# Kernel optimization log

Measured on AMD Instinct MI355X. Metric: run time of the kernel, lower is better.

## Reference

```python
import jax, jax.numpy as jnp
import numpy as np

BN_EPS = 1e-5


def conv1x1(x, W, b):
    # x: [B, Cin, N], W: [Cout, Cin], b: [Cout]
    return jnp.einsum('oc,bcn->bon', W, x) + b[None, :, None]


def bn(x, p):
    # p: [4, C] rows = gamma, beta, running_mean, running_var (inference BN)
    g, be, m, v = p[0], p[1], p[2], p[3]
    inv = jax.lax.rsqrt(v + BN_EPS)
    return (x - m[None, :, None]) * (g * inv)[None, :, None] + be[None, :, None]


def conv_bn_relu(x, W, b, p):
    return jax.nn.relu(bn(conv1x1(x, W, b), p))


def _make_params(key, cout, cin):
    k1, k2 = jax.random.split(key)
    W = jax.random.normal(k1, (cout, cin), jnp.float32) * (1.0 / np.sqrt(cin))
    b = jax.random.normal(k2, (cout,), jnp.float32) * 0.01
    p = jnp.stack([jnp.ones(cout), jnp.zeros(cout), jnp.zeros(cout), jnp.ones(cout)]).astype(jnp.float32)
    return W, b, p


def setup_inputs() -> dict:
    key = jax.random.key(0)
    ks = jax.random.split(key, 16)
    B, N, S, D1, D2 = 2, 16384, 4096, 128, 256
    Cin, C, Cm = D1 + D2 + 13, 128, 128  # 397, out_channel, mlp[0]
    inp = {
        'xyz1': jax.random.normal(ks[0], (B, N, 3), jnp.float32),
        'xyz2': jax.random.normal(ks[1], (B, S, 3), jnp.float32),
        'points1': jax.random.normal(ks[2], (B, D1, N), jnp.float32),
        'points2': jax.random.normal(ks[3], (B, D2, S), jnp.float32),
        'last_pred': jax.random.normal(ks[4], (B, S, 13), jnp.float32),
    }
    inp['fuse_W'], inp['fuse_b'], inp['fuse_bn'] = _make_params(ks[5], C, Cin)
    inp['ext1_W'], inp['ext1_b'], inp['ext1_bn'] = _make_params(ks[6], C, C)
    inp['ext2_W'], inp['ext2_b'], inp['ext2_bn'] = _make_params(ks[7], C, C)
    inp['pred1_W'], inp['pred1_b'], inp['pred1_bn'] = _make_params(ks[8], Cm, C)
    inp['pred2_W'], inp['pred2_b'], inp['pred2_bn'] = _make_params(ks[9], 13, Cm)
    return inp


def _forward(xyz1, xyz2, points1, points2, last_pred,
             fuse_W, fuse_b, fuse_bn, ext1_W, ext1_b, ext1_bn,
             ext2_W, ext2_b, ext2_bn, pred1_W, pred1_b, pred1_bn,
             pred2_W, pred2_b, pred2_bn):
    B, N, _ = xyz1.shape
    p1 = jnp.transpose(points1, (0, 2, 1))  # [B, N, D1]
    p2 = jnp.transpose(points2, (0, 2, 1))  # [B, S, D2]
    # squared distances [B, N, S]
    dists = (jnp.sum(xyz1 ** 2, -1)[:, :, None]
             + jnp.sum(xyz2 ** 2, -1)[:, None, :]
             - 2.0 * jnp.einsum('bnc,bsc->bns', xyz1, xyz2))
    # 3 smallest distances (partial top-k instead of full sort; same math)
    neg_d3, idx = jax.lax.top_k(-dists, 3)  # [B, N, 3]
    d3 = -neg_d3
    recip = 1.0 / (d3 + 1e-8)
    weight = recip / jnp.sum(recip, axis=2, keepdims=True)  # [B, N, 3]
    bidx = jnp.arange(B)[:, None, None]
    interp_pts = jnp.sum(p2[bidx, idx] * weight[..., None], axis=2)        # [B, N, D2]
    interp_pred = jnp.sum(last_pred[bidx, idx] * weight[..., None], axis=2)  # [B, N, 13]
    new_points = jnp.transpose(jnp.concatenate([p1, interp_pts, interp_pred], axis=-1), (0, 2, 1))  # [B, Cin, N]
    # fuse
    x = conv_bn_relu(new_points, fuse_W, fuse_b, fuse_bn)
    # extraction: one ConvBNReLURes1D block (groups=1, res_expansion=1)
    h = conv_bn_relu(x, ext1_W, ext1_b, ext1_bn)
    x = jax.nn.relu(bn(conv1x1(h, ext2_W, ext2_b), ext2_bn) + x)  # [B, C, N]
    new_points_out = x
    # prediction head (dropout is identity in eval mode)
    feat = conv_bn_relu(x, pred1_W, pred1_b, pred1_bn)
    pred = conv_bn_relu(feat, pred2_W, pred2_b, pred2_bn)
    return (new_points_out,
            jnp.transpose(feat, (0, 2, 1)),
            jnp.transpose(pred, (0, 2, 1)))


def reference(xyz1, xyz2, points1, points2, last_pred,
              fuse_W, fuse_b, fuse_bn, ext1_W, ext1_b, ext1_bn,
              ext2_W, ext2_b, ext2_bn, pred1_W, pred1_b, pred1_bn,
              pred2_W, pred2_b, pred2_bn):
    return _forward(xyz1, xyz2, points1, points2, last_pred,
                    fuse_W, fuse_b, fuse_bn, ext1_W, ext1_b, ext1_bn,
                    ext2_W, ext2_b, ext2_bn, pred1_W, pred1_b, pred1_bn,
                    pred2_W, pred2_b, pred2_bn)
```

## Files before the change

### kernel.cpp

```cpp
#include <hip/hip_runtime.h>
#include <stdint.h>

#define B_   2
#define N_   16384
#define S_   4096
#define D2_  256
#define CIN_ 397
#define KP_  416
#define C_   128
#define OC_  13
#define NCHUNK_ 16
#define CHS_ (S_ / NCHUNK_)
#define NCAND_ (NCHUNK_ * 3)
#define XBI_P 296

typedef unsigned short u16;
typedef unsigned int u32;
typedef short s16x8 __attribute__((ext_vector_type(8)));
typedef float f32x4 __attribute__((ext_vector_type(4)));

#define MFMA16(a, b, c) __builtin_amdgcn_mfma_f32_16x16x32_bf16((a), (b), (c), 0, 0, 0)

__device__ __forceinline__ float b2f(u16 h) {
  union { unsigned int u; float f; } v; v.u = ((unsigned int)h) << 16; return v.f;
}
__device__ __forceinline__ u16 f2b(float f) {
  union { float f; unsigned int u; } v; v.f = f;
  unsigned int r = v.u + 0x7fffu + ((v.u >> 16) & 1u);
  return (u16)(r >> 16);
}

__global__ void prep_kernel(const float* __restrict__ fW, const float* __restrict__ fb,
                            const float* __restrict__ fbn,
                            const float* __restrict__ e1W, const float* __restrict__ e1b,
                            const float* __restrict__ e1bn,
                            const float* __restrict__ e2W, const float* __restrict__ e2b,
                            const float* __restrict__ e2bn,
                            const float* __restrict__ p1W, const float* __restrict__ p1b,
                            const float* __restrict__ p1bn,
                            const float* __restrict__ p2W, const float* __restrict__ p2b,
                            const float* __restrict__ p2bn,
                            u16* __restrict__ Wf, u16* __restrict__ W1o,
                            u16* __restrict__ W2o, u16* __restrict__ W3o,
                            u16* __restrict__ Wp2, float* __restrict__ st) {
  int tid = blockIdx.x * 256 + threadIdx.x;
  int stride = gridDim.x * 256;
  for (int i = tid; i < 128 * KP_; i += stride) {
    int m = i / KP_, k = i - m * KP_;
    Wf[i] = (k < CIN_) ? f2b(fW[m * CIN_ + k]) : (u16)0;
  }
  for (int i = tid; i < 128 * 128; i += stride) {
    W1o[i] = f2b(e1W[i]);
    W2o[i] = f2b(e2W[i]);
    W3o[i] = f2b(p1W[i]);
  }
  for (int i = tid; i < 16 * 128; i += stride) {
    int m = i >> 7;
    Wp2[i] = (m < OC_) ? f2b(p2W[i]) : (u16)0;
  }
  for (int i = tid; i < 5 * 128; i += stride) {
    int sg = i >> 7, c = i & 127;
    const float* bn; const float* bc; int Cc = 128;
    switch (sg) {
      case 0: bn = fbn;  bc = fb;  break;
      case 1: bn = e1bn; bc = e1b; break;
      case 2: bn = e2bn; bc = e2b; break;
      case 3: bn = p1bn; bc = p1b; break;
      default: bn = p2bn; bc = p2b; Cc = OC_; break;
    }
    float s = 0.f, t = 0.f;
    if (c < Cc) {
      float g  = bn[0 * Cc + c], be = bn[1 * Cc + c];
      float mu = bn[2 * Cc + c], vv = bn[3 * Cc + c];
      float inv = 1.0f / sqrtf(vv + 1e-5f);
      s = g * inv;
      t = (bc[c] - mu) * s + be;
    }
    st[sg * 256 + c] = s;
    st[sg * 256 + 128 + c] = t;
  }
}

__global__ void transpose_f2b_kernel(const float* __restrict__ in, u16* __restrict__ out,
                                     int C, int S, int opitch) {
  __shared__ float tile[64][65];
  int b = blockIdx.z;
  int s0 = blockIdx.x * 64, c0 = blockIdx.y * 64;
  const float* ip = in + (size_t)b * C * S;
  u16* op = out + (size_t)b * S * opitch;
  int tr = threadIdx.x >> 4;
  int tc4 = (threadIdx.x & 15) * 4;
#pragma unroll
  for (int r = 0; r < 64; r += 16) {
    float4 v = *(const float4*)(ip + (size_t)(c0 + tr + r) * S + s0 + tc4);
    tile[tr + r][tc4 + 0] = v.x;
    tile[tr + r][tc4 + 1] = v.y;
    tile[tr + r][tc4 + 2] = v.z;
    tile[tr + r][tc4 + 3] = v.w;
  }
  __syncthreads();
#pragma unroll
  for (int r = 0; r < 64; r += 16) {
    ushort4 v;
    v.x = f2b(tile[tc4 + 0][tr + r]);
    v.y = f2b(tile[tc4 + 1][tr + r]);
    v.z = f2b(tile[tc4 + 2][tr + r]);
    v.w = f2b(tile[tc4 + 3][tr + r]);
    *(ushort4*)(op + (size_t)(s0 + tr + r) * opitch + c0 + tc4) = v;
  }
}

__global__ __launch_bounds__(256) void knn_scan_kernel(
    const float* __restrict__ xyz1, const float* __restrict__ xyz2,
    u16* __restrict__ cand) {
  __shared__ float4 pts[CHS_];
  int b = blockIdx.z;
  int chunk = blockIdx.x;
  int s0 = chunk * CHS_;
  int tid = threadIdx.x;
  const float* x2 = xyz2 + ((size_t)b * S_ + s0) * 3;
  {
    float xx = x2[tid * 3], yy = x2[tid * 3 + 1], zz = x2[tid * 3 + 2];
    pts[tid] = make_float4(xx, yy, zz, fmaf(xx, xx, fmaf(yy, yy, zz * zz)));
  }
  __syncthreads();
  int n = blockIdx.y * 256 + tid;
  const float* x1 = xyz1 + ((size_t)b * N_ + n) * 3;
  float ax = x1[0], ay = x1[1], az = x1[2];
  float n1 = fmaf(ax, ax, fmaf(ay, ay, az * az));
  u32 k0 = 0xFFFFFFFFu, k1 = 0xFFFFFFFFu, k2 = 0xFFFFFFFFu;
#pragma unroll 8
  for (int s = 0; s < CHS_; ++s) {
    float4 p = pts[s];
    float dot = fmaf(ax, p.x, fmaf(ay, p.y, az * p.z));
    float d = fmaf(-2.f, dot, n1 + p.w);
    d = fmaxf(d, 0.f);
    u32 key = (__float_as_uint(d) & 0xFFFFFF00u) | (u32)s;
    u32 nk0 = min(k0, key);
    u32 nk1 = min(k1, max(k0, key));
    u32 nk2 = min(k2, max(k1, key));
    k0 = nk0; k1 = nk1; k2 = nk2;
  }
  u16* co = cand + ((size_t)(b * N_ + n)) * NCAND_ + chunk * 3;
  co[0] = (u16)((k0 & 0xFFu) + s0);
  co[1] = (u16)((k1 & 0xFFu) + s0);
  co[2] = (u16)((k2 & 0xFFu) + s0);
}

__global__ void knn_merge_kernel(const float* __restrict__ xyz1,
                                 const float* __restrict__ xyz2,
                                 const u16* __restrict__ cand,
                                 float* __restrict__ wout, int* __restrict__ iout) {
#pragma clang fp contract(off)
  int q = blockIdx.x * 256 + threadIdx.x;
  int b = q >> 14;
  const u16* ci = cand + (size_t)q * NCAND_;
  const float* x1 = xyz1 + (size_t)q * 3;
  double ax = x1[0], ay = x1[1], az = x1[2];
  double n1 = (ax * ax + ay * ay) + az * az;
  const float* x2b = xyz2 + (size_t)b * S_ * 3;
  double D0 = 1e300, D1 = 1e300, D2v = 1e300;
  int I0 = 2147483647, I1 = 2147483647, I2 = 2147483647;
  for (int j = 0; j < NCAND_; ++j) {
    int i = ci[j];
    const float* p = x2b + (size_t)i * 3;
    double px = p[0], py = p[1], pz = p[2];
    double n2 = (px * px + py * py) + pz * pz;
    double dot = (ax * px + ay * py) + az * pz;
    double d = (n1 + n2) - 2.0 * dot;
    if ((d < D2v) || (d == D2v && i < I2)) {
      if ((d < D1) || (d == D1 && i < I1)) {
        D2v = D1; I2 = I1;
        if ((d < D0) || (d == D0 && i < I0)) { D1 = D0; I1 = I0; D0 = d; I0 = i; }
        else                                  { D1 = d; I1 = i; }
      } else { D2v = d; I2 = i; }
    }
  }
  double r0 = 1.0 / (D0 + 1e-8);
  double r1 = 1.0 / (D1 + 1e-8);
  double r2 = 1.0 / (D2v + 1e-8);
  double sum = (r0 + r1) + r2;
  size_t o = (size_t)q * 3;
  wout[o + 0] = (float)(r0 / sum);
  wout[o + 1] = (float)(r1 / sum);
  wout[o + 2] = (float)(r2 / sum);
  iout[o + 0] = I0; iout[o + 1] = I1; iout[o + 2] = I2;
}

__device__ __forceinline__ void gemm_lds128(const u16* __restrict__ W, const u16* xb,
                                            int l15, int lq, int nbase, f32x4 acc[8][2]) {
#pragma unroll
  for (int mt = 0; mt < 8; ++mt) {
    acc[mt][0] = (f32x4){0.f, 0.f, 0.f, 0.f};
    acc[mt][1] = (f32x4){0.f, 0.f, 0.f, 0.f};
  }
  for (int ks = 0; ks < 4; ++ks) {
    int ko = ks * 32 + lq * 8;
    s16x8 b0 = *(const s16x8*)(xb + (nbase + l15) * 136 + ko);
    s16x8 b1 = *(const s16x8*)(xb + (nbase + 16 + l15) * 136 + ko);
#pragma unroll
    for (int mt = 0; mt < 8; ++mt) {
      s16x8 a = *(const s16x8*)(W + (size_t)(mt * 16 + l15) * 128 + ko);
      acc[mt][0] = MFMA16(a, b0, acc[mt][0]);
      acc[mt][1] = MFMA16(a, b1, acc[mt][1]);
    }
  }
}

__global__ __launch_bounds__(256) void mega_kernel(
    const u16* __restrict__ npT, const u16* __restrict__ p2t,
    const float* __restrict__ last_pred,
    const float* __restrict__ knw, const int* __restrict__ kni,
    const u16* __restrict__ Wf,
    const u16* __restrict__ W1, const u16* __restrict__ W2,
    const u16* __restrict__ W3, const u16* __restrict__ Wp2,
    const float* __restrict__ st, float* __restrict__ out) {
  __shared__ u16 xb0[128 * 136];
  __shared__ u16 xb1[128 * 136];
  __shared__ u16 xbi[128 * XBI_P];
  int b = blockIdx.y;
  int n0 = blockIdx.x * 128;
  int tid = threadIdx.x;
  int wv = tid >> 6, lane = tid & 63;
  int l15 = lane & 15, lq = lane >> 4;
  int nbase = wv * 32;
  f32x4 acc[8][2];

  {
    const float* lpb = last_pred + (size_t)b * S_ * OC_;
    const u16* p2b = p2t + (size_t)b * S_ * D2_;
#pragma unroll 1
    for (int i = 0; i < 32; ++i) {
      int p = nbase + i;
      size_t o = ((size_t)(b * N_ + n0 + p)) * 3;
      float w0 = knw[o], w1 = knw[o + 1], w2 = knw[o + 2];
      int i0 = kni[o], i1 = kni[o + 1], i2 = kni[o + 2];
      ushort4 a0 = *(const ushort4*)(p2b + (size_t)i0 * D2_ + lane * 4);
      ushort4 a1 = *(const ushort4*)(p2b + (size_t)i1 * D2_ + lane * 4);
      ushort4 a2 = *(const ushort4*)(p2b + (size_t)i2 * D2_ + lane * 4);
      ushort4 v;
      v.x = f2b((w0 * b2f(a0.x) + w1 * b2f(a1.x)) + w2 * b2f(a2.x));
      v.y = f2b((w0 * b2f(a0.y) + w1 * b2f(a1.y)) + w2 * b2f(a2.y));
      v.z = f2b((w0 * b2f(a0.z) + w1 * b2f(a1.z)) + w2 * b2f(a2.z));
      v.w = f2b((w0 * b2f(a0.w) + w1 * b2f(a1.w)) + w2 * b2f(a2.w));
      *(ushort4*)(&xbi[p * XBI_P + lane * 4]) = v;
      if (lane < 32) {
        u16 pv = 0;
        if (lane < OC_) {
          pv = f2b((w0 * lpb[i0 * OC_ + lane] + w1 * lpb[i1 * OC_ + lane])
                   + w2 * lpb[i2 * OC_ + lane]);
        }
        xbi[p * XBI_P + 256 + lane] = pv;
      }
    }
  }

#pragma unroll
  for (int mt = 0; mt < 8; ++mt) {
    acc[mt][0] = (f32x4){0.f, 0.f, 0.f, 0.f};
    acc[mt][1] = (f32x4){0.f, 0.f, 0.f, 0.f};
  }
  {
    const u16* brow0 = npT + ((size_t)(b * N_ + n0 + nbase + l15)) * 128;
    const u16* brow1 = brow0 + (size_t)16 * 128;
#pragma unroll 1
    for (int ks = 0; ks < 4; ++ks) {
      int ko = ks * 32 + lq * 8;
      s16x8 bf0 = *(const s16x8*)(brow0 + ko);
      s16x8 bf1 = *(const s16x8*)(brow1 + ko);
#pragma unroll
      for (int mt = 0; mt < 8; ++mt) {
        s16x8 a = *(const s16x8*)(Wf + (size_t)(mt * 16 + l15) * KP_ + ko);
        acc[mt][0] = MFMA16(a, bf0, acc[mt][0]);
        acc[mt][1] = MFMA16(a, bf1, acc[mt][1]);
      }
    }
#pragma unroll 1
    for (int ks = 0; ks < 9; ++ks) {
      int kk = ks * 32 + lq * 8;
      s16x8 bf0 = *(const s16x8*)(&xbi[(nbase + l15) * XBI_P + kk]);
      s16x8 bf1 = *(const s16x8*)(&xbi[(nbase + 16 + l15) * XBI_P + kk]);
#pragma unroll
      for (int mt = 0; mt < 8; ++mt) {
        s16x8 a = *(const s16x8*)(Wf + (size_t)(mt * 16 + l15) * KP_ + 128 + kk);
        acc[mt][0] = MFMA16(a, bf0, acc[mt][0]);
        acc[mt][1] = MFMA16(a, bf1, acc[mt][1]);
      }
    }
  }
#pragma unroll
  for (int mt = 0; mt < 8; ++mt) {
    f32x4 sc = *(const f32x4*)(st + 0 * 256 + mt * 16 + lq * 4);
    f32x4 bi = *(const f32x4*)(st + 0 * 256 + 128 + mt * 16 + lq * 4);
#pragma unroll
    for (int nt = 0; nt < 2; ++nt) {
      int n_l = nbase + nt * 16 + l15;
      ushort4 v;
      v.x = f2b(fmaxf(acc[mt][nt][0] * sc[0] + bi[0], 0.f));
      v.y = f2b(fmaxf(acc[mt][nt][1] * sc[1] + bi[1], 0.f));
      v.z = f2b(fmaxf(acc[mt][nt][2] * sc[2] + bi[2], 0.f));
      v.w = f2b(fmaxf(acc[mt][nt][3] * sc[3] + bi[3], 0.f));
      *(ushort4*)(&xb0[n_l * 136 + mt * 16 + lq * 4]) = v;
    }
  }
  __syncthreads();

  gemm_lds128(W1, xb0, l15, lq, nbase, acc);
#pragma unroll
  for (int mt = 0; mt < 8; ++mt) {
    f32x4 sc = *(const f32x4*)(st + 1 * 256 + mt * 16 + lq * 4);
    f32x4 bi = *(const f32x4*)(st + 1 * 256 + 128 + mt * 16 + lq * 4);
#pragma unroll
    for (int nt = 0; nt < 2; ++nt) {
      int n_l = nbase + nt * 16 + l15;
      ushort4 v;
      v.x = f2b(fmaxf(acc[mt][nt][0] * sc[0] + bi[0], 0.f));
      v.y = f2b(fmaxf(acc[mt][nt][1] * sc[1] + bi[1], 0.f));
      v.z = f2b(fmaxf(acc[mt][nt][2] * sc[2] + bi[2], 0.f));
      v.w = f2b(fmaxf(acc[mt][nt][3] * sc[3] + bi[3], 0.f));
      *(ushort4*)(&xb1[n_l * 136 + mt * 16 + lq * 4]) = v;
    }
  }
  __syncthreads();

  gemm_lds128(W2, xb1, l15, lq, nbase, acc);
#pragma unroll
  for (int mt = 0; mt < 8; ++mt) {
    f32x4 sc = *(const f32x4*)(st + 2 * 256 + mt * 16 + lq * 4);
    f32x4 bi = *(const f32x4*)(st + 2 * 256 + 128 + mt * 16 + lq * 4);
#pragma unroll
    for (int nt = 0; nt < 2; ++nt) {
      int n_l = nbase + nt * 16 + l15;
      int n_g = n0 + n_l;
      ushort4 xp = *(const ushort4*)(&xb0[n_l * 136 + mt * 16 + lq * 4]);
      float v0 = fmaxf(acc[mt][nt][0] * sc[0] + bi[0] + b2f(xp.x), 0.f);
      float v1 = fmaxf(acc[mt][nt][1] * sc[1] + bi[1] + b2f(xp.y), 0.f);
      float v2 = fmaxf(acc[mt][nt][2] * sc[2] + bi[2] + b2f(xp.z), 0.f);
      float v3 = fmaxf(acc[mt][nt][3] * sc[3] + bi[3] + b2f(xp.w), 0.f);
      ushort4 v;
      v.x = f2b(v0); v.y = f2b(v1); v.z = f2b(v2); v.w = f2b(v3);
      *(ushort4*)(&xb0[n_l * 136 + mt * 16 + lq * 4]) = v;
      int m = mt * 16 + lq * 4;
      out[((size_t)(b * C_ + m + 0)) * N_ + n_g] = v0;
      out[((size_t)(b * C_ + m + 1)) * N_ + n_g] = v1;
      out[((size_t)(b * C_ + m + 2)) * N_ + n_g] = v2;
      out[((size_t)(b * C_ + m + 3)) * N_ + n_g] = v3;
    }
  }
  __syncthreads();

  gemm_lds128(W3, xb0, l15, lq, nbase, acc);
  {
    float* out1 = out + (size_t)B_ * C_ * N_;
#pragma unroll
    for (int mt = 0; mt < 8; ++mt) {
      f32x4 sc = *(const f32x4*)(st + 3 * 256 + mt * 16 + lq * 4);
      f32x4 bi = *(const f32x4*)(st + 3 * 256 + 128 + mt * 16 + lq * 4);
#pragma unroll
      for (int nt = 0; nt < 2; ++nt) {
        int n_l = nbase + nt * 16 + l15;
        int n_g = n0 + n_l;
        float v0 = fmaxf(acc[mt][nt][0] * sc[0] + bi[0], 0.f);
        float v1 = fmaxf(acc[mt][nt][1] * sc[1] + bi[1], 0.f);
        float v2 = fmaxf(acc[mt][nt][2] * sc[2] + bi[2], 0.f);
        float v3 = fmaxf(acc[mt][nt][3] * sc[3] + bi[3], 0.f);
        ushort4 v;
        v.x = f2b(v0); v.y = f2b(v1); v.z = f2b(v2); v.w = f2b(v3);
        *(ushort4*)(&xb1[n_l * 136 + mt * 16 + lq * 4]) = v;
        float4 o4 = make_float4(v0, v1, v2, v3);
        *(float4*)(out1 + ((size_t)(b * N_ + n_g)) * 128 + mt * 16 + lq * 4) = o4;
      }
    }
  }
  __syncthreads();

  {
    f32x4 a2[2];
    a2[0] = (f32x4){0.f, 0.f, 0.f, 0.f};
    a2[1] = (f32x4){0.f, 0.f, 0.f, 0.f};
    for (int ks = 0; ks < 4; ++ks) {
      int ko = ks * 32 + lq * 8;
      s16x8 b0 = *(const s16x8*)(&xb1[(nbase + l15) * 136 + ko]);
      s16x8 b1 = *(const s16x8*)(&xb1[(nbase + 16 + l15) * 136 + ko]);
      s16x8 a = *(const s16x8*)(Wp2 + (size_t)l15 * 128 + ko);
      a2[0] = MFMA16(a, b0, a2[0]);
      a2[1] = MFMA16(a, b1, a2[1]);
    }
    float* out2 = out + (size_t)B_ * C_ * N_ + (size_t)B_ * N_ * 128;
    f32x4 sc = *(const f32x4*)(st + 4 * 256 + lq * 4);
    f32x4 bi = *(const f32x4*)(st + 4 * 256 + 128 + lq * 4);
#pragma unroll
    for (int nt = 0; nt < 2; ++nt) {
      int n_g = n0 + nbase + nt * 16 + l15;
#pragma unroll
      for (int r = 0; r < 4; ++r) {
        int m = lq * 4 + r;
        if (m < OC_) {
          out2[((size_t)(b * N_ + n_g)) * OC_ + m] =
              fmaxf(a2[nt][r] * sc[r] + bi[r], 0.f);
        }
      }
    }
  }
}

extern "C" void kernel_launch(void* const* d_in, const int* in_sizes, int n_in,
                              void* d_out, int out_size, void* d_ws, size_t ws_size,
                              hipStream_t stream) {
  const float* xyz1      = (const float*)d_in[0];
  const float* xyz2      = (const float*)d_in[1];
  const float* points1   = (const float*)d_in[2];
  const float* points2   = (const float*)d_in[3];
  const float* last_pred = (const float*)d_in[4];
  const float* fuse_W    = (const float*)d_in[5];
  const float* fuse_b    = (const float*)d_in[6];
  const float* fuse_bn   = (const float*)d_in[7];
  const float* ext1_W    = (const float*)d_in[8];
  const float* ext1_b    = (const float*)d_in[9];
  const float* ext1_bn   = (const float*)d_in[10];
  const float* ext2_W    = (const float*)d_in[11];
  const float* ext2_b    = (const float*)d_in[12];
  const float* ext2_bn   = (const float*)d_in[13];
  const float* pred1_W   = (const float*)d_in[14];
  const float* pred1_b   = (const float*)d_in[15];
  const float* pred1_bn  = (const float*)d_in[16];
  const float* pred2_W   = (const float*)d_in[17];
  const float* pred2_b   = (const float*)d_in[18];
  const float* pred2_bn  = (const float*)d_in[19];

  char* ws = (char*)d_ws;
  u16*   npT  = (u16*)(ws + 0);
  u16*   p2t  = (u16*)(ws + 8388608);
  float* knw  = (float*)(ws + 12582912);
  int*   kni  = (int*)(ws + 12976128);
  u16*   cand = (u16*)(ws + 13369344);
  u16*   Wf   = (u16*)(ws + 16515072);
  u16*   W1   = (u16*)(ws + 16621568);
  u16*   W2   = (u16*)(ws + 16654336);
  u16*   W3   = (u16*)(ws + 16687104);
  u16*   Wp2  = (u16*)(ws + 16719872);
  float* st   = (float*)(ws + 16723968);

  prep_kernel<<<dim3(64), dim3(256), 0, stream>>>(
      fuse_W, fuse_b, fuse_bn, ext1_W, ext1_b, ext1_bn, ext2_W, ext2_b, ext2_bn,
      pred1_W, pred1_b, pred1_bn, pred2_W, pred2_b, pred2_bn,
      Wf, W1, W2, W3, Wp2, st);

  transpose_f2b_kernel<<<dim3(N_ / 64, 128 / 64, B_), dim3(256), 0, stream>>>(
      points1, npT, 128, N_, 128);
  transpose_f2b_kernel<<<dim3(S_ / 64, 256 / 64, B_), dim3(256), 0, stream>>>(
      points2, p2t, 256, S_, 256);

  knn_scan_kernel<<<dim3(NCHUNK_, N_ / 256, B_), dim3(256), 0, stream>>>(
      xyz1, xyz2, cand);
  knn_merge_kernel<<<dim3(B_ * N_ / 256), dim3(256), 0, stream>>>(
      xyz1, xyz2, cand, knw, kni);

  mega_kernel<<<dim3(N_ / 128, B_), dim3(256), 0, stream>>>(
      npT, p2t, last_pred, knw, kni, Wf, W1, W2, W3, Wp2, st, (float*)d_out);
}
```

Measured before the change: 238.2 us.

## Shrink mega kernel tile to 32 points, merge setup kernels, split KNN merge

Retiles the fused MLP kernel from 128 to 32 points per block. Each wave now owns two 16-row output-channel tiles instead of 32 points, which cuts accumulator registers and LDS per block and launches four times more blocks with launch bounds asking for 4 blocks per CU. The weight prep and the two transpose kernels are merged into one launch. The KNN merge keeps two independent top-3 lists to give more instruction-level parallelism. The trade-off is that each weight element is reused across fewer points, so weights are loaded from L2 more often per point.

```diff
diff --git a/kernel.cpp b/kernel.cpp
--- a/kernel.cpp
+++ b/kernel.cpp
@@ -30,21 +30,65 @@
   return (u16)(r >> 16);
 }
 
-__global__ void prep_kernel(const float* __restrict__ fW, const float* __restrict__ fb,
-                            const float* __restrict__ fbn,
-                            const float* __restrict__ e1W, const float* __restrict__ e1b,
-                            const float* __restrict__ e1bn,
-                            const float* __restrict__ e2W, const float* __restrict__ e2b,
-                            const float* __restrict__ e2bn,
-                            const float* __restrict__ p1W, const float* __restrict__ p1b,
-                            const float* __restrict__ p1bn,
-                            const float* __restrict__ p2W, const float* __restrict__ p2b,
-                            const float* __restrict__ p2bn,
-                            u16* __restrict__ Wf, u16* __restrict__ W1o,
-                            u16* __restrict__ W2o, u16* __restrict__ W3o,
-                            u16* __restrict__ Wp2, float* __restrict__ st) {
-  int tid = blockIdx.x * 256 + threadIdx.x;
-  int stride = gridDim.x * 256;
+__device__ __forceinline__ void transpose_body(
+    const float* __restrict__ in, u16* __restrict__ out,
+    int C, int S, int opitch, int b, int s0, int c0,
+    float (*tile)[65], int tr, int tc4) {
+  const float* ip = in + (size_t)b * C * S;
+  u16* op = out + (size_t)b * S * opitch;
+#pragma unroll
+  for (int r = 0; r < 64; r += 16) {
+    float4 v = *(const float4*)(ip + (size_t)(c0 + tr + r) * S + s0 + tc4);
+    tile[tr + r][tc4 + 0] = v.x;
+    tile[tr + r][tc4 + 1] = v.y;
+    tile[tr + r][tc4 + 2] = v.z;
+    tile[tr + r][tc4 + 3] = v.w;
+  }
+  __syncthreads();
+#pragma unroll
+  for (int r = 0; r < 64; r += 16) {
+    ushort4 v;
+    v.x = f2b(tile[tc4 + 0][tr + r]);
+    v.y = f2b(tile[tc4 + 1][tr + r]);
+    v.z = f2b(tile[tc4 + 2][tr + r]);
+    v.w = f2b(tile[tc4 + 3][tr + r]);
+    *(ushort4*)(op + (size_t)(s0 + tr + r) * opitch + c0 + tc4) = v;
+  }
+}
+
+__global__ __launch_bounds__(256) void setup_kernel(
+    const float* __restrict__ points1, const float* __restrict__ points2,
+    const float* __restrict__ fW, const float* __restrict__ fb,
+    const float* __restrict__ fbn,
+    const float* __restrict__ e1W, const float* __restrict__ e1b,
+    const float* __restrict__ e1bn,
+    const float* __restrict__ e2W, const float* __restrict__ e2b,
+    const float* __restrict__ e2bn,
+    const float* __restrict__ p1W, const float* __restrict__ p1b,
+    const float* __restrict__ p1bn,
+    const float* __restrict__ p2W, const float* __restrict__ p2b,
+    const float* __restrict__ p2bn,
+    u16* __restrict__ npT, u16* __restrict__ p2t,
+    u16* __restrict__ Wf, u16* __restrict__ W1o,
+    u16* __restrict__ W2o, u16* __restrict__ W3o,
+    u16* __restrict__ Wp2, float* __restrict__ st) {
+  __shared__ float tile[64][65];
+  int id = blockIdx.x;
+  int tr = threadIdx.x >> 4;
+  int tc4 = (threadIdx.x & 15) * 4;
+  if (id < 1024) {
+    int sx = id & 255, sy = (id >> 8) & 1, b = id >> 9;
+    transpose_body(points1, npT, 128, N_, 128, b, sx * 64, sy * 64, tile, tr, tc4);
+    return;
+  }
+  if (id < 1536) {
+    int id2 = id - 1024;
+    int sx = id2 & 63, sy = (id2 >> 6) & 3, b = id2 >> 8;
+    transpose_body(points2, p2t, 256, S_, 256, b, sx * 64, sy * 64, tile, tr, tc4);
+    return;
+  }
+  int tid = (id - 1536) * 256 + threadIdx.x;
+  int stride = 64 * 256;
   for (int i = tid; i < 128 * KP_; i += stride) {
     int m = i / KP_, k = i - m * KP_;
     Wf[i] = (k < CIN_) ? f2b(fW[m * CIN_ + k]) : (u16)0;
@@ -78,35 +122,6 @@
     }
     st[sg * 256 + c] = s;
     st[sg * 256 + 128 + c] = t;
-  }
-}
-
-__global__ void transpose_f2b_kernel(const float* __restrict__ in, u16* __restrict__ out,
-                                     int C, int S, int opitch) {
-  __shared__ float tile[64][65];
-  int b = blockIdx.z;
-  int s0 = blockIdx.x * 64, c0 = blockIdx.y * 64;
-  const float* ip = in + (size_t)b * C * S;
-  u16* op = out + (size_t)b * S * opitch;
-  int tr = threadIdx.x >> 4;
-  int tc4 = (threadIdx.x & 15) * 4;
-#pragma unroll
-  for (int r = 0; r < 64; r += 16) {
-    float4 v = *(const float4*)(ip + (size_t)(c0 + tr + r) * S + s0 + tc4);
-    tile[tr + r][tc4 + 0] = v.x;
-    tile[tr + r][tc4 + 1] = v.y;
-    tile[tr + r][tc4 + 2] = v.z;
-    tile[tr + r][tc4 + 3] = v.w;
-  }
-  __syncthreads();
-#pragma unroll
-  for (int r = 0; r < 64; r += 16) {
-    ushort4 v;
-    v.x = f2b(tile[tc4 + 0][tr + r]);
-    v.y = f2b(tile[tc4 + 1][tr + r]);
-    v.z = f2b(tile[tc4 + 2][tr + r]);
-    v.w = f2b(tile[tc4 + 3][tr + r]);
-    *(ushort4*)(op + (size_t)(s0 + tr + r) * opitch + c0 + tc4) = v;
   }
 }
 
@@ -147,6 +162,18 @@
   co[2] = (u16)((k2 & 0xFFu) + s0);
 }
 
+__device__ __forceinline__ void ins3(double d, int i,
+                                     double& D0, double& D1, double& D2,
+                                     int& I0, int& I1, int& I2) {
+  if ((d < D2) || (d == D2 && i < I2)) {
+    if ((d < D1) || (d == D1 && i < I1)) {
+      D2 = D1; I2 = I1;
+      if ((d < D0) || (d == D0 && i < I0)) { D1 = D0; I1 = I0; D0 = d; I0 = i; }
+      else                                  { D1 = d; I1 = i; }
+    } else { D2 = d; I2 = i; }
+  }
+}
+
 __global__ void knn_merge_kernel(const float* __restrict__ xyz1,
                                  const float* __restrict__ xyz2,
                                  const u16* __restrict__ cand,
@@ -159,55 +186,59 @@
   double ax = x1[0], ay = x1[1], az = x1[2];
   double n1 = (ax * ax + ay * ay) + az * az;
   const float* x2b = xyz2 + (size_t)b * S_ * 3;
-  double D0 = 1e300, D1 = 1e300, D2v = 1e300;
-  int I0 = 2147483647, I1 = 2147483647, I2 = 2147483647;
-  for (int j = 0; j < NCAND_; ++j) {
-    int i = ci[j];
-    const float* p = x2b + (size_t)i * 3;
-    double px = p[0], py = p[1], pz = p[2];
-    double n2 = (px * px + py * py) + pz * pz;
-    double dot = (ax * px + ay * py) + az * pz;
-    double d = (n1 + n2) - 2.0 * dot;
-    if ((d < D2v) || (d == D2v && i < I2)) {
-      if ((d < D1) || (d == D1 && i < I1)) {
-        D2v = D1; I2 = I1;
-        if ((d < D0) || (d == D0 && i < I0)) { D1 = D0; I1 = I0; D0 = d; I0 = i; }
-        else                                  { D1 = d; I1 = i; }
-      } else { D2v = d; I2 = i; }
-    }
-  }
-  double r0 = 1.0 / (D0 + 1e-8);
-  double r1 = 1.0 / (D1 + 1e-8);
-  double r2 = 1.0 / (D2v + 1e-8);
+  double A0 = 1e300, A1 = 1e300, A2 = 1e300;
+  int Ia0 = 2147483647, Ia1 = 2147483647, Ia2 = 2147483647;
+  double Bd0 = 1e300, Bd1 = 1e300, Bd2 = 1e300;
+  int Ib0 = 2147483647, Ib1 = 2147483647, Ib2 = 2147483647;
+  for (int j = 0; j < NCAND_ / 2; ++j) {
+    int ia = ci[2 * j], ib = ci[2 * j + 1];
+    const float* pa = x2b + (size_t)ia * 3;
+    const float* pb = x2b + (size_t)ib * 3;
+    double pax = pa[0], pay = pa[1], paz = pa[2];
+    double pbx = pb[0], pby = pb[1], pbz = pb[2];
+    double na = (pax * pax + pay * pay) + paz * paz;
+    double nb = (pbx * pbx + pby * pby) + pbz * pbz;
+    double da = (n1 + na) - 2.0 * ((ax * pax + ay * pay) + az * paz);
+    double db = (n1 + nb) - 2.0 * ((ax * pbx + ay * pby) + az * pbz);
+    ins3(da, ia, A0, A1, A2, Ia0, Ia1, Ia2);
+    ins3(db, ib, Bd0, Bd1, Bd2, Ib0, Ib1, Ib2);
+  }
+  ins3(Bd0, Ib0, A0, A1, A2, Ia0, Ia1, Ia2);
+  ins3(Bd1, Ib1, A0, A1, A2, Ia0, Ia1, Ia2);
+  ins3(Bd2, Ib2, A0, A1, A2, Ia0, Ia1, Ia2);
+  double r0 = 1.0 / (A0 + 1e-8);
+  double r1 = 1.0 / (A1 + 1e-8);
+  double r2 = 1.0 / (A2 + 1e-8);
   double sum = (r0 + r1) + r2;
   size_t o = (size_t)q * 3;
   wout[o + 0] = (float)(r0 / sum);
   wout[o + 1] = (float)(r1 / sum);
   wout[o + 2] = (float)(r2 / sum);
-  iout[o + 0] = I0; iout[o + 1] = I1; iout[o + 2] = I2;
-}
-
-__device__ __forceinline__ void gemm_lds128(const u16* __restrict__ W, const u16* xb,
-                                            int l15, int lq, int nbase, f32x4 acc[8][2]) {
-#pragma unroll
-  for (int mt = 0; mt < 8; ++mt) {
-    acc[mt][0] = (f32x4){0.f, 0.f, 0.f, 0.f};
-    acc[mt][1] = (f32x4){0.f, 0.f, 0.f, 0.f};
-  }
+  iout[o + 0] = Ia0; iout[o + 1] = Ia1; iout[o + 2] = Ia2;
+}
+
+__device__ __forceinline__ void gemm32(const u16* __restrict__ W, const u16* xb,
+                                       int l15, int lq, int wv, f32x4 acc[2][2]) {
+#pragma unroll
+  for (int mtl = 0; mtl < 2; ++mtl) {
+    acc[mtl][0] = (f32x4){0.f, 0.f, 0.f, 0.f};
+    acc[mtl][1] = (f32x4){0.f, 0.f, 0.f, 0.f};
+  }
+#pragma unroll
   for (int ks = 0; ks < 4; ++ks) {
     int ko = ks * 32 + lq * 8;
-    s16x8 b0 = *(const s16x8*)(xb + (nbase + l15) * 136 + ko);
-    s16x8 b1 = *(const s16x8*)(xb + (nbase + 16 + l15) * 136 + ko);
-#pragma unroll
-    for (int mt = 0; mt < 8; ++mt) {
-      s16x8 a = *(const s16x8*)(W + (size_t)(mt * 16 + l15) * 128 + ko);
-      acc[mt][0] = MFMA16(a, b0, acc[mt][0]);
-      acc[mt][1] = MFMA16(a, b1, acc[mt][1]);
-    }
-  }
-}
-
-__global__ __launch_bounds__(256) void mega_kernel(
+    s16x8 b0 = *(const s16x8*)(xb + l15 * 136 + ko);
+    s16x8 b1 = *(const s16x8*)(xb + (16 + l15) * 136 + ko);
+#pragma unroll
+    for (int mtl = 0; mtl < 2; ++mtl) {
+      s16x8 a = *(const s16x8*)(W + (size_t)((wv * 2 + mtl) * 16 + l15) * 128 + ko);
+      acc[mtl][0] = MFMA16(a, b0, acc[mtl][0]);
+      acc[mtl][1] = MFMA16(a, b1, acc[mtl][1]);
+    }
+  }
+}
+
+__global__ __launch_bounds__(256, 4) void mega_kernel(
     const u16* __restrict__ npT, const u16* __restrict__ p2t,
     const float* __restrict__ last_pred,
     const float* __restrict__ knw, const int* __restrict__ kni,
@@ -215,23 +246,22 @@
     const u16* __restrict__ W1, const u16* __restrict__ W2,
     const u16* __restrict__ W3, const u16* __restrict__ Wp2,
     const float* __restrict__ st, float* __restrict__ out) {
-  __shared__ u16 xb0[128 * 136];
-  __shared__ u16 xb1[128 * 136];
-  __shared__ u16 xbi[128 * XBI_P];
+  __shared__ u16 xb0[32 * 136];
+  __shared__ u16 xb1[32 * 136];
+  __shared__ u16 xbi[32 * XBI_P];
   int b = blockIdx.y;
-  int n0 = blockIdx.x * 128;
+  int n0 = blockIdx.x * 32;
   int tid = threadIdx.x;
   int wv = tid >> 6, lane = tid & 63;
   int l15 = lane & 15, lq = lane >> 4;
-  int nbase = wv * 32;
-  f32x4 acc[8][2];
+  f32x4 acc[2][2];
 
   {
     const float* lpb = last_pred + (size_t)b * S_ * OC_;
     const u16* p2b = p2t + (size_t)b * S_ * D2_;
-#pragma unroll 1
-    for (int i = 0; i < 32; ++i) {
-      int p = nbase + i;
+#pragma unroll 2
+    for (int i = 0; i < 8; ++i) {
+      int p = wv * 8 + i;
       size_t o = ((size_t)(b * N_ + n0 + p)) * 3;
       float w0 = knw[o], w1 = knw[o + 1], w2 = knw[o + 2];
       int i0 = kni[o], i1 = kni[o + 1], i2 = kni[o + 2];
@@ -254,14 +284,15 @@
       }
     }
   }
-
-#pragma unroll
-  for (int mt = 0; mt < 8; ++mt) {
-    acc[mt][0] = (f32x4){0.f, 0.f, 0.f, 0.f};
-    acc[mt][1] = (f32x4){0.f, 0.f, 0.f, 0.f};
+  __syncthreads();
+
+#pragma unroll
+  for (int mtl = 0; mtl < 2; ++mtl) {
+    acc[mtl][0] = (f32x4){0.f, 0.f, 0.f, 0.f};
+    acc[mtl][1] = (f32x4){0.f, 0.f, 0.f, 0.f};
   }
   {
-    const u16* brow0 = npT + ((size_t)(b * N_ + n0 + nbase + l15)) * 128;
+    const u16* brow0 = npT + ((size_t)(b * N_ + n0 + l15)) * 128;
     const u16* brow1 = brow0 + (size_t)16 * 128;
 #pragma unroll 1
     for (int ks = 0; ks < 4; ++ks) {
@@ -269,136 +300,133 @@
       s16x8 bf0 = *(const s16x8*)(brow0 + ko);
       s16x8 bf1 = *(const s16x8*)(brow1 + ko);
 #pragma unroll
-      for (int mt = 0; mt < 8; ++mt) {
-        s16x8 a = *(const s16x8*)(Wf + (size_t)(mt * 16 + l15) * KP_ + ko);
-        acc[mt][0] = MFMA16(a, bf0, acc[mt][0]);
-        acc[mt][1] = MFMA16(a, bf1, acc[mt][1]);
+      for (int mtl = 0; mtl < 2; ++mtl) {
+        s16x8 a = *(const s16x8*)(Wf + (size_t)((wv * 2 + mtl) * 16 + l15) * KP_ + ko);
+        acc[mtl][0] = MFMA16(a, bf0, acc[mtl][0]);
+        acc[mtl][1] = MFMA16(a, bf1, acc[mtl][1]);
       }
     }
 #pragma unroll 1
     for (int ks = 0; ks < 9; ++ks) {
       int kk = ks * 32 + lq * 8;
-      s16x8 bf0 = *(const s16x8*)(&xbi[(nbase + l15) * XBI_P + kk]);
-      s16x8 bf1 = *(const s16x8*)(&xbi[(nbase + 16 + l15) * XBI_P + kk]);
-#pragma unroll
-      for (int mt = 0; mt < 8; ++mt) {
-        s16x8 a = *(const s16x8*)(Wf + (size_t)(mt * 16 + l15) * KP_ + 128 + kk);
-        acc[mt][0] = MFMA16(a, bf0, acc[mt][0]);
-        acc[mt][1] = MFMA16(a, bf1, acc[mt][1]);
+      s16x8 bf0 = *(const s16x8*)(&xbi[l15 * XBI_P + kk]);
+      s16x8 bf1 = *(const s16x8*)(&xbi[(16 + l15) * XBI_P + kk]);
+#pragma unroll
+      for (int mtl = 0; mtl < 2; ++mtl) {
+        s16x8 a = *(const s16x8*)(Wf + (size_t)((wv * 2 + mtl) * 16 + l15) * KP_ + 128 + kk);
+        acc[mtl][0] = MFMA16(a, bf0, acc[mtl][0]);
+        acc[mtl][1] = MFMA16(a, bf1, acc[mtl][1]);
       }
     }
   }
 #pragma unroll
-  for (int mt = 0; mt < 8; ++mt) {
-    f32x4 sc = *(const f32x4*)(st + 0 * 256 + mt * 16 + lq * 4);
-    f32x4 bi = *(const f32x4*)(st + 0 * 256 + 128 + mt * 16 + lq * 4);
+  for (int mtl = 0; mtl < 2; ++mtl) {
+    int m4 = (wv * 2 + mtl) * 16 + lq * 4;
+    f32x4 sc = *(const f32x4*)(st + 0 * 256 + m4);
+    f32x4 bi = *(const f32x4*)(st + 0 * 256 + 128 + m4);
 #pragma unroll
     for (int nt = 0; nt < 2; ++nt) {
-      int n_l = nbase + nt * 16 + l15;
+      int n_l = nt * 16 + l15;
       ushort4 v;
-      v.x = f2b(fmaxf(acc[mt][nt][0] * sc[0] + bi[0], 0.f));
-      v.y = f2b(fmaxf(acc[mt][nt][1] * sc[1] + bi[1], 0.f));
-      v.z = f2b(fmaxf(acc[mt][nt][2] * sc[2] + bi[2], 0.f));
-      v.w = f2b(fmaxf(acc[mt][nt][3] * sc[3] + bi[3], 0.f));
-      *(ushort4*)(&xb0[n_l * 136 + mt * 16 + lq * 4]) = v;
-    }
-  }
-  __syncthreads();
-
-  gemm_lds128(W1, xb0, l15, lq, nbase, acc);
-#pragma unroll
-  for (int mt = 0; mt < 8; ++mt) {
-    f32x4 sc = *(const f32x4*)(st + 1 * 256 + mt * 16 + lq * 4);
-    f32x4 bi = *(const f32x4*)(st + 1 * 256 + 128 + mt * 16 + lq * 4);
+      v.x = f2b(fmaxf(acc[mtl][nt][0] * sc[0] + bi[0], 0.f));
+      v.y = f2b(fmaxf(acc[mtl][nt][1] * sc[1] + bi[1], 0.f));
+      v.z = f2b(fmaxf(acc[mtl][nt][2] * sc[2] + bi[2], 0.f));
+      v.w = f2b(fmaxf(acc[mtl][nt][3] * sc[3] + bi[3], 0.f));
+      *(ushort4*)(&xb0[n_l * 136 + m4]) = v;
+    }
+  }
+  __syncthreads();
+
+  gemm32(W1, xb0, l15, lq, wv, acc);
+#pragma unroll
+  for (int mtl = 0; mtl < 2; ++mtl) {
+    int m4 = (wv * 2 + mtl) * 16 + lq * 4;
+    f32x4 sc = *(const f32x4*)(st + 1 * 256 + m4);
+    f32x4 bi = *(const f32x4*)(st + 1 * 256 + 128 + m4);
 #pragma unroll
     for (int nt = 0; nt < 2; ++nt) {
-      int n_l = nbase + nt * 16 + l15;
+      int n_l = nt * 16 + l15;
       ushort4 v;
-      v.x = f2b(fmaxf(acc[mt][nt][0] * sc[0] + bi[0], 0.f));
-      v.y = f2b(fmaxf(acc[mt][nt][1] * sc[1] + bi[1], 0.f));
-      v.z = f2b(fmaxf(acc[mt][nt][2] * sc[2] + bi[2], 0.f));
-      v.w = f2b(fmaxf(acc[mt][nt][3] * sc[3] + bi[3], 0.f));
-      *(ushort4*)(&xb1[n_l * 136 + mt * 16 + lq * 4]) = v;
-    }
-  }
-  __syncthreads();
-
-  gemm_lds128(W2, xb1, l15, lq, nbase, acc);
-#pragma unroll
-  for (int mt = 0; mt < 8; ++mt) {
-    f32x4 sc = *(const f32x4*)(st + 2 * 256 + mt * 16 + lq * 4);
-    f32x4 bi = *(const f32x4*)(st + 2 * 256 + 128 + mt * 16 + lq * 4);
+      v.x = f2b(fmaxf(acc[mtl][nt][0] * sc[0] + bi[0], 0.f));
+      v.y = f2b(fmaxf(acc[mtl][nt][1] * sc[1] + bi[1], 0.f));
+      v.z = f2b(fmaxf(acc[mtl][nt][2] * sc[2] + bi[2], 0.f));
+      v.w = f2b(fmaxf(acc[mtl][nt][3] * sc[3] + bi[3], 0.f));
+      *(ushort4*)(&xb1[n_l * 136 + m4]) = v;
+    }
+  }
+  __syncthreads();
+
+  gemm32(W2, xb1, l15, lq, wv, acc);
+#pragma unroll
+  for (int mtl = 0; mtl < 2; ++mtl) {
+    int m4 = (wv * 2 + mtl) * 16 + lq * 4;
+    f32x4 sc = *(const f32x4*)(st + 2 * 256 + m4);
+    f32x4 bi = *(const f32x4*)(st + 2 * 256 + 128 + m4);
 #pragma unroll
     for (int nt = 0; nt < 2; ++nt) {
-      int n_l = nbase + nt * 16 + l15;
+      int n_l = nt * 16 + l15;
       int n_g = n0 + n_l;
-      ushort4 xp = *(const ushort4*)(&xb0[n_l * 136 + mt * 16 + lq * 4]);
-      float v0 = fmaxf(acc[mt][nt][0] * sc[0] + bi[0] + b2f(xp.x), 0.f);
-      float v1 = fmaxf(acc[mt][nt][1] * sc[1] + bi[1] + b2f(xp.y), 0.f);
-      float v2 = fmaxf(acc[mt][nt][2] * sc[2] + bi[2] + b2f(xp.z), 0.f);
-      float v3 = fmaxf(acc[mt][nt][3] * sc[3] + bi[3] + b2f(xp.w), 0.f);
+      ushort4 xp = *(const ushort4*)(&xb0[n_l * 136 + m4]);
+      float v0 = fmaxf(acc[mtl][nt][0] * sc[0] + bi[0] + b2f(xp.x), 0.f);
+      float v1 = fmaxf(acc[mtl][nt][1] * sc[1] + bi[1] + b2f(xp.y), 0.f);
+      float v2 = fmaxf(acc[mtl][nt][2] * sc[2] + bi[2] + b2f(xp.z), 0.f);
+      float v3 = fmaxf(acc[mtl][nt][3] * sc[3] + bi[3] + b2f(xp.w), 0.f);
       ushort4 v;
       v.x = f2b(v0); v.y = f2b(v1); v.z = f2b(v2); v.w = f2b(v3);
-      *(ushort4*)(&xb0[n_l * 136 + mt * 16 + lq * 4]) = v;
-      int m = mt * 16 + lq * 4;
-      out[((size_t)(b * C_ + m + 0)) * N_ + n_g] = v0;
-      out[((size_t)(b * C_ + m + 1)) * N_ + n_g] = v1;
-      out[((size_t)(b * C_ + m + 2)) * N_ + n_g] = v2;
-      out[((size_t)(b * C_ + m + 3)) * N_ + n_g] = v3;
-    }
-  }
-  __syncthreads();
-
-  gemm_lds128(W3, xb0, l15, lq, nbase, acc);
+      *(ushort4*)(&xb0[n_l * 136 + m4]) = v;
+      out[((size_t)(b * C_ + m4 + 0)) * N_ + n_g] = v0;
+      out[((size_t)(b * C_ + m4 + 1)) * N_ + n_g] = v1;
+      out[((size_t)(b * C_ + m4 + 2)) * N_ + n_g] = v2;
+      out[((size_t)(b * C_ + m4 + 3)) * N_ + n_g] = v3;
+    }
+  }
+  __syncthreads();
+
+  gemm32(W3, xb0, l15, lq, wv, acc);
   {
     float* out1 = out + (size_t)B_ * C_ * N_;
 #pragma unroll
-    for (int mt = 0; mt < 8; ++mt) {
-      f32x4 sc = *(const f32x4*)(st + 3 * 256 + mt * 16 + lq * 4);
-      f32x4 bi = *(const f32x4*)(st + 3 * 256 + 128 + mt * 16 + lq * 4);
+    for (int mtl = 0; mtl < 2; ++mtl) {
+      int m4 = (wv * 2 + mtl) * 16 + lq * 4;
+      f32x4 sc = *(const f32x4*)(st + 3 * 256 + m4);
+      f32x4 bi = *(const f32x4*)(st + 3 * 256 + 128 + m4);
 #pragma unroll
       for (int nt = 0; nt < 2; ++nt) {
-        int n_l = nbase + nt * 16 + l15;
+        int n_l = nt * 16 + l15;
         int n_g = n0 + n_l;
-        float v0 = fmaxf(acc[mt][nt][0] * sc[0] + bi[0], 0.f);
-        float v1 = fmaxf(acc[mt][nt][1] * sc[1] + bi[1], 0.f);
-        float v2 = fmaxf(acc[mt][nt][2] * sc[2] + bi[2], 0.f);
-        float v3 = fmaxf(acc[mt][nt][3] * sc[3] + bi[3], 0.f);
+        float v0 = fmaxf(acc[mtl][nt][0] * sc[0] + bi[0], 0.f);
+        float v1 = fmaxf(acc[mtl][nt][1] * sc[1] + bi[1], 0.f);
+        float v2 = fmaxf(acc[mtl][nt][2] * sc[2] + bi[2], 0.f);
+        float v3 = fmaxf(acc[mtl][nt][3] * sc[3] + bi[3], 0.f);
         ushort4 v;
         v.x = f2b(v0); v.y = f2b(v1); v.z = f2b(v2); v.w = f2b(v3);
-        *(ushort4*)(&xb1[n_l * 136 + mt * 16 + lq * 4]) = v;
+        *(ushort4*)(&xb1[n_l * 136 + m4]) = v;
         float4 o4 = make_float4(v0, v1, v2, v3);
-        *(float4*)(out1 + ((size_t)(b * N_ + n_g)) * 128 + mt * 16 + lq * 4) = o4;
+        *(float4*)(out1 + ((size_t)(b * N_ + n_g)) * 128 + m4) = o4;
       }
     }
   }
   __syncthreads();
 
-  {
-    f32x4 a2[2];
-    a2[0] = (f32x4){0.f, 0.f, 0.f, 0.f};
-    a2[1] = (f32x4){0.f, 0.f, 0.f, 0.f};
+  if (wv < 2) {
+    f32x4 a2 = (f32x4){0.f, 0.f, 0.f, 0.f};
+#pragma unroll
     for (int ks = 0; ks < 4; ++ks) {
       int ko = ks * 32 + lq * 8;
-      s16x8 b0 = *(const s16x8*)(&xb1[(nbase + l15) * 136 + ko]);
-      s16x8 b1 = *(const s16x8*)(&xb1[(nbase + 16 + l15) * 136 + ko]);
+      s16x8 b0 = *(const s16x8*)(&xb1[(wv * 16 + l15) * 136 + ko]);
       s16x8 a = *(const s16x8*)(Wp2 + (size_t)l15 * 128 + ko);
-      a2[0] = MFMA16(a, b0, a2[0]);
-      a2[1] = MFMA16(a, b1, a2[1]);
+      a2 = MFMA16(a, b0, a2);
     }
     float* out2 = out + (size_t)B_ * C_ * N_ + (size_t)B_ * N_ * 128;
     f32x4 sc = *(const f32x4*)(st + 4 * 256 + lq * 4);
     f32x4 bi = *(const f32x4*)(st + 4 * 256 + 128 + lq * 4);
-#pragma unroll
-    for (int nt = 0; nt < 2; ++nt) {
-      int n_g = n0 + nbase + nt * 16 + l15;
-#pragma unroll
-      for (int r = 0; r < 4; ++r) {
-        int m = lq * 4 + r;
-        if (m < OC_) {
-          out2[((size_t)(b * N_ + n_g)) * OC_ + m] =
-              fmaxf(a2[nt][r] * sc[r] + bi[r], 0.f);
-        }
+    int n_g = n0 + wv * 16 + l15;
+#pragma unroll
+    for (int r = 0; r < 4; ++r) {
+      int m = lq * 4 + r;
+      if (m < OC_) {
+        out2[((size_t)(b * N_ + n_g)) * OC_ + m] =
+            fmaxf(a2[r] * sc[r] + bi[r], 0.f);
       }
     }
   }
@@ -441,21 +469,17 @@
   u16*   Wp2  = (u16*)(ws + 16719872);
   float* st   = (float*)(ws + 16723968);
 
-  prep_kernel<<<dim3(64), dim3(256), 0, stream>>>(
+  setup_kernel<<<dim3(1600), dim3(256), 0, stream>>>(
+      points1, points2,
       fuse_W, fuse_b, fuse_bn, ext1_W, ext1_b, ext1_bn, ext2_W, ext2_b, ext2_bn,
       pred1_W, pred1_b, pred1_bn, pred2_W, pred2_b, pred2_bn,
-      Wf, W1, W2, W3, Wp2, st);
-
-  transpose_f2b_kernel<<<dim3(N_ / 64, 128 / 64, B_), dim3(256), 0, stream>>>(
-      points1, npT, 128, N_, 128);
-  transpose_f2b_kernel<<<dim3(S_ / 64, 256 / 64, B_), dim3(256), 0, stream>>>(
-      points2, p2t, 256, S_, 256);
+      npT, p2t, Wf, W1, W2, W3, Wp2, st);
 
   knn_scan_kernel<<<dim3(NCHUNK_, N_ / 256, B_), dim3(256), 0, stream>>>(
       xyz1, xyz2, cand);
   knn_merge_kernel<<<dim3(B_ * N_ / 256), dim3(256), 0, stream>>>(
       xyz1, xyz2, cand, knw, kni);
 
-  mega_kernel<<<dim3(N_ / 128, B_), dim3(256), 0, stream>>>(
+  mega_kernel<<<dim3(N_ / 32, B_), dim3(256), 0, stream>>>(
       npT, p2t, last_pred, knw, kni, Wf, W1, W2, W3, Wp2, st, (float*)d_out);
 }
```

After: 236.2 us. About the same (-0.9%).
